# Kernel tuning notes

Measured on AMD Instinct MI355X. Metric: run time of the kernel, lower is better.

The kernel has to match this reference:

```python
import jax, jax.numpy as jnp
import numpy as np
import math

B, S, D, H = 2, 2048, 1024, 16
DK = D // H


def setup_inputs() -> dict:
    key = jax.random.key(0)
    ks = jax.random.split(key, 10)
    sc = 1.0 / math.sqrt(D)
    inp = {
        "Q_input": jax.random.normal(ks[0], (B, S, D), dtype=jnp.float32),
        "Wq_w": jax.random.normal(ks[1], (D, D), dtype=jnp.float32) * sc,
        "Wq_b": jnp.zeros((D,), dtype=jnp.float32),
        "Wk_w": jax.random.normal(ks[2], (D, D), dtype=jnp.float32) * sc,
        "Wk_b": jnp.zeros((D,), dtype=jnp.float32),
        "Wv_w": jax.random.normal(ks[3], (D, D), dtype=jnp.float32) * sc,
        "Wv_b": jnp.zeros((D,), dtype=jnp.float32),
        "Wo_w": jax.random.normal(ks[4], (D, D), dtype=jnp.float32) * sc,
        "Wo_b": jnp.zeros((D,), dtype=jnp.float32),
        # causal mask, broadcast over batch and heads: [1,1,S,S]
        "mask": jnp.tril(jnp.ones((S, S), dtype=jnp.int32))[None, None],
    }
    return inp


def reference(Q_input, Wq_w, Wq_b, Wk_w, Wk_b, Wv_w, Wv_b, Wo_w, Wo_b, mask):
    b, s, _ = Q_input.shape
    # linear projections (torch Linear: x @ W^T + b)
    Q = Q_input @ Wq_w.T + Wq_b
    K = Q_input @ Wk_w.T + Wk_b
    V = Q_input @ Wv_w.T + Wv_b
    # [b, h, s, dk]
    Q = Q.reshape(b, s, H, DK).transpose(0, 2, 1, 3)
    K = K.reshape(b, s, H, DK).transpose(0, 2, 1, 3)
    V = V.reshape(b, s, H, DK).transpose(0, 2, 1, 3)
    scores = jnp.einsum("bhqd,bhkd->bhqk", Q, K) / math.sqrt(DK)
    scores = jnp.where(mask == 0, jnp.float32(-1e9), scores)
    weights = jax.nn.softmax(scores, axis=-1)
    attn = jnp.einsum("bhqk,bhkd->bhqd", weights, V)
    attn = attn.transpose(0, 2, 1, 3).reshape(b, s, D)
    return attn @ Wo_w.T + Wo_b
```

## Files before the change

### kernel.cpp

```cpp
#include <hip/hip_runtime.h>
#include <hip/hip_bf16.h>
#include <cstdint>

typedef __attribute__((ext_vector_type(8))) short short8;
typedef __attribute__((ext_vector_type(4))) float f32x4;
typedef __attribute__((ext_vector_type(2))) unsigned int uint2v;
typedef unsigned short ushort_t;

#define S_LEN 2048
#define D_DIM 1024
#define NH 16
#define DK 64
#define BATCH 2
#define M_ROWS (BATCH * S_LEN)
#define BK 32

__device__ inline ushort_t f2bf(float f) {
    union { float f; uint32_t u; } v; v.f = f;
    uint32_t r = v.u + 0x7fffu + ((v.u >> 16) & 1u);
    return (ushort_t)(r >> 16);
}

__device__ __forceinline__ ushort_t bfc(float f) {
    __hip_bfloat16 h = __float2bfloat16(f);
    return __builtin_bit_cast(ushort_t, h);
}

__device__ __forceinline__ float bf2f(ushort_t u) {
    return __uint_as_float(((uint32_t)u) << 16);
}

__device__ __forceinline__ float fexp2(float x) {
#if __has_builtin(__builtin_amdgcn_exp2f)
    return __builtin_amdgcn_exp2f(x);
#else
    return exp2f(x);
#endif
}
__device__ __forceinline__ float frcp(float x) {
#if __has_builtin(__builtin_amdgcn_rcpf)
    return __builtin_amdgcn_rcpf(x);
#else
    return 1.0f / x;
#endif
}

__device__ __forceinline__ void glds16(const ushort_t* g, ushort_t* l) {
    __builtin_amdgcn_global_load_lds(
        (const __attribute__((address_space(1))) uint32_t*)g,
        (__attribute__((address_space(3))) uint32_t*)l,
        16, 0, 0);
}

#if __has_builtin(__builtin_amdgcn_permlane16_swap) && __has_builtin(__builtin_amdgcn_permlane32_swap)
#define HAS_PLSWAP 1
#else
#define HAS_PLSWAP 0
#endif

__device__ __forceinline__ float red_max4(float x) {
#if HAS_PLSWAP
    uint2v a = __builtin_amdgcn_permlane16_swap(__float_as_uint(x), __float_as_uint(x), false, false);
    float y = fmaxf(__uint_as_float(a.x), __uint_as_float(a.y));
    uint2v b = __builtin_amdgcn_permlane32_swap(__float_as_uint(y), __float_as_uint(y), false, false);
    return fmaxf(__uint_as_float(b.x), __uint_as_float(b.y));
#else
    x = fmaxf(x, __shfl_xor(x, 16));
    return fmaxf(x, __shfl_xor(x, 32));
#endif
}
__device__ __forceinline__ float red_sum4(float x) {
#if HAS_PLSWAP
    uint2v a = __builtin_amdgcn_permlane16_swap(__float_as_uint(x), __float_as_uint(x), false, false);
    float y = __uint_as_float(a.x) + __uint_as_float(a.y);
    uint2v b = __builtin_amdgcn_permlane32_swap(__float_as_uint(y), __float_as_uint(y), false, false);
    return __uint_as_float(b.x) + __uint_as_float(b.y);
#else
    x += __shfl_xor(x, 16);
    return x + __shfl_xor(x, 32);
#endif
}

__device__ __forceinline__ void route_p(const uint32_t wp[4][2], int ks, int lane, uint32_t F[4]) {
#if HAS_PLSWAP
    uint32_t U0 = wp[2 * ks][0],     U1 = wp[2 * ks][1];
    uint32_t V0 = wp[2 * ks + 1][0], V1 = wp[2 * ks + 1][1];
    uint2v t, pa0, pa1, pb0, pb1;
    t = __builtin_amdgcn_permlane32_swap(U0, U0, false, false);
    pa0 = __builtin_amdgcn_permlane16_swap(U0, t.y, false, false);
    t = __builtin_amdgcn_permlane32_swap(U1, U1, false, false);
    pa1 = __builtin_amdgcn_permlane16_swap(U1, t.y, false, false);
    t = __builtin_amdgcn_permlane32_swap(V0, V0, false, false);
    pb0 = __builtin_amdgcn_permlane16_swap(t.x, V0, false, false);
    t = __builtin_amdgcn_permlane32_swap(V1, V1, false, false);
    pb1 = __builtin_amdgcn_permlane16_swap(t.x, V1, false, false);
    bool lo = lane < 32;
    F[0] = lo ? pa0.x : pb0.x;
    F[1] = lo ? pa1.x : pb1.x;
    F[2] = lo ? pa0.y : pb0.y;
    F[3] = lo ? pa1.y : pb1.y;
#else
    int q = lane & 15, g = lane >> 4;
#pragma unroll
    for (int m = 0; m < 4; m++) {
        int src = 16 * (2 * (g & 1) + (m >> 1)) + q;
        uint32_t xa = (uint32_t)__shfl((int)wp[2 * ks][m & 1], src);
        uint32_t xb = (uint32_t)__shfl((int)wp[2 * ks + 1][m & 1], src);
        F[m] = (g < 2) ? xa : xb;
    }
#endif
}

__global__ void cvt_bf16(const float* __restrict__ in, ushort_t* __restrict__ out, int n4) {
    int i = blockIdx.x * blockDim.x + threadIdx.x;
    int stride = gridDim.x * blockDim.x;
    for (int idx = i; idx < n4; idx += stride) {
        float4 v = ((const float4*)in)[idx];
        ushort4 o;
        o.x = f2bf(v.x); o.y = f2bf(v.y); o.z = f2bf(v.z); o.w = f2bf(v.w);
        ((ushort4*)out)[idx] = o;
    }
}

__global__ void cvt_w3(const float* __restrict__ wq, const float* __restrict__ wk,
                       const float* __restrict__ wv, ushort_t* __restrict__ wqkv) {
    const int seg = (D_DIM * D_DIM) / 4;
    int i = blockIdx.x * blockDim.x + threadIdx.x;
    int stride = gridDim.x * blockDim.x;
    for (int idx = i; idx < 3 * seg; idx += stride) {
        int sel = idx >> 18;
        int id = idx & (seg - 1);
        const float* src = sel == 0 ? wq : (sel == 1 ? wk : wv);
        float4 v = ((const float4*)src)[id];
        ushort4 o;
        o.x = f2bf(v.x); o.y = f2bf(v.y); o.z = f2bf(v.z); o.w = f2bf(v.w);
        ((ushort4*)wqkv)[sel * seg + id] = o;
    }
}

template<int MODE, int BMt, int BNt>
__global__ __launch_bounds__(256) void gemm_bt(const ushort_t* __restrict__ A,
                                               const ushort_t* __restrict__ Bw,
                                               const float* __restrict__ b0,
                                               const float* __restrict__ b1,
                                               const float* __restrict__ b2,
                                               void* __restrict__ C0,
                                               void* __restrict__ C1,
                                               void* __restrict__ C2,
                                               int M, int N, int K) {
    constexpr int FM = BMt / 32, FN = BNt / 32;
    constexpr int ACH = BMt / 64, BCH = BNt / 64;
    __shared__ ushort_t As[BMt * BK];
    __shared__ ushort_t Bs[BNt * BK];
    int tid = threadIdx.x;
    int lane = tid & 63;
    int w = tid >> 6;
    int wr = w >> 1, wc = w & 1;
    int nwg = gridDim.x;
    int bx = (blockIdx.x & 7) * (nwg >> 3) + (blockIdx.x >> 3);
    int ntile = N / BNt;
    int m0 = (bx / ntile) * BMt;
    int n0 = (bx % ntile) * BNt;
    int lr = lane & 15;
    int lk = (lane >> 4) * 8;
    int srow = lane >> 2;
    int scol = (lane & 3) * 8;

    f32x4 acc[FM][FN] = {};

    for (int kt = 0; kt < K; kt += BK) {
        __syncthreads();
#pragma unroll
        for (int c = 0; c < ACH; c++)
            glds16(&A[(size_t)(m0 + w * (BMt / 4) + c * 16 + srow) * K + kt + scol],
                   &As[(w * (BMt / 4) + c * 16) * BK]);
#pragma unroll
        for (int c = 0; c < BCH; c++)
            glds16(&Bw[(size_t)(n0 + w * (BNt / 4) + c * 16 + srow) * K + kt + scol],
                   &Bs[(w * (BNt / 4) + c * 16) * BK]);
        __syncthreads();

        short8 af[FM], bf[FN];
#pragma unroll
        for (int f = 0; f < FM; f++)
            af[f] = *(const short8*)&As[(wr * (BMt / 2) + f * 16 + lr) * BK + lk];
#pragma unroll
        for (int f = 0; f < FN; f++)
            bf[f] = *(const short8*)&Bs[(wc * (BNt / 2) + f * 16 + lr) * BK + lk];
#pragma unroll
        for (int i = 0; i < FM; i++)
#pragma unroll
            for (int j = 0; j < FN; j++)
                acc[i][j] = __builtin_amdgcn_mfma_f32_16x16x32_bf16(af[i], bf[j], acc[i][j], 0, 0, 0);
    }

    int r0 = (lane >> 4) * 4;
#pragma unroll
    for (int j = 0; j < FN; j++) {
        int ncol = n0 + wc * (BNt / 2) + j * 16 + lr;
        if (MODE == 2) {
            float bv = b0[ncol];
#pragma unroll
            for (int i = 0; i < FM; i++) {
                int mbase = m0 + wr * (BMt / 2) + i * 16 + r0;
#pragma unroll
                for (int r = 0; r < 4; r++)
                    ((float*)C0)[(size_t)(mbase + r) * N + ncol] = acc[i][j][r] + bv;
            }
        } else {
            int sel = n0 >> 10;
            const float* bp = sel == 0 ? b0 : (sel == 1 ? b1 : b2);
            int nc = ncol & 1023;
            float bv = bp[nc];
            int hh = nc >> 6, dk = nc & 63;
            ushort_t* Co = (ushort_t*)(sel == 0 ? C0 : (sel == 1 ? C1 : C2));
#pragma unroll
            for (int i = 0; i < FM; i++) {
                int mbase = m0 + wr * (BMt / 2) + i * 16 + r0;
                int bb = mbase >> 11, ss = mbase & 2047;
                if (sel == 2) {
                    ushort4 pk;
                    pk.x = f2bf(acc[i][j][0] + bv);
                    pk.y = f2bf(acc[i][j][1] + bv);
                    pk.z = f2bf(acc[i][j][2] + bv);
                    pk.w = f2bf(acc[i][j][3] + bv);
                    size_t idx = ((size_t)(bb * NH + hh) * DK + dk) * S_LEN + ss;
                    *(ushort4*)&Co[idx] = pk;
                } else {
#pragma unroll
                    for (int r = 0; r < 4; r++) {
                        size_t idx = ((size_t)(bb * NH + hh) * S_LEN + (ss + r)) * DK + dk;
                        Co[idx] = f2bf(acc[i][j][r] + bv);
                    }
                }
            }
        }
    }
}

#define CSC 0.1803368801f

__device__ const unsigned char JTAB[40] = {
    23,22,21,20,19,18,17,16,
    31,31,30,28,29,26,27,15,
    24,25,30,28,29,27,26,14,
    24,11, 9,10, 8,25,12,13,
     0, 1, 2, 4, 6, 5, 7, 3};
__device__ const unsigned char KTAB[40] = {
     9, 9, 9, 9, 9, 9, 9, 9,
     0, 1, 0, 0, 0, 0, 1, 9,
     0, 0, 1, 1, 1, 0, 1, 9,
     1, 9, 9, 9, 9, 1, 9, 9,
     9, 9, 9, 9, 9, 9, 9, 9};

__global__ __launch_bounds__(256) void attn_fwd(const ushort_t* __restrict__ Q,
                                                const ushort_t* __restrict__ K,
                                                const ushort_t* __restrict__ Vt,
                                                ushort_t* __restrict__ Oa,
                                                float2* __restrict__ ml,
                                                float* __restrict__ Pd) {
    __shared__ ushort_t Ks[2][64 * 64];
    __shared__ ushort_t Vs[2][64 * 64];

    int tid = threadIdx.x;
    int lane = tid & 63;
    int w = tid >> 6;
    int bh = blockIdx.x;
    int yy = blockIdx.y;
    int j = JTAB[yy];
    int kk = KTAB[yy];
    int nt = j + 1;
    int half = (nt + 1) >> 1;
    int t0 = (kk == 1) ? half : 0;
    int t1 = (kk == 0) ? half : nt;
    int cnt = t1 - t0;
    int off = yy % cnt;
    size_t base = (size_t)bh * S_LEN * DK;
    int q0 = j * 64;

    int lr = lane & 15;
    int lk = (lane >> 4) * 8;
    int g16 = (lane >> 4) * 16;
    int r0 = (lane >> 4) * 4;
    int wq = w * 16 + lr;

    auto swz = [](int row, int cb) { return (row * 128 + (cb ^ ((row & 7) << 4))) >> 1; };

    short8 qf0 = *(const short8*)&Q[base + (size_t)(q0 + wq) * DK + lk];
    short8 qf1 = *(const short8*)&Q[base + (size_t)(q0 + wq) * DK + 32 + lk];

    f32x4 o[4] = {};
    float mrowL = -1e30f, lrow = 0.f;

    int sr = tid >> 3;
    int scb = (tid & 7) * 16;
    int sce = (tid & 7) * 8;

    {
        int tf = t0 + off;
        *(uint4*)&Ks[0][swz(sr, scb)]      = *(const uint4*)&K [base + (size_t)(tf * 64 + sr) * DK + sce];
        *(uint4*)&Ks[0][swz(sr + 32, scb)] = *(const uint4*)&K [base + (size_t)(tf * 64 + sr + 32) * DK + sce];
        *(uint4*)&Vs[0][swz(sr, scb)]      = *(const uint4*)&Vt[base + (size_t)sr * S_LEN + tf * 64 + sce];
        *(uint4*)&Vs[0][swz(sr + 32, scb)] = *(const uint4*)&Vt[base + (size_t)(sr + 32) * S_LEN + tf * 64 + sce];
    }
    __syncthreads();

    int cur = 0;
    for (int s = 0; s < cnt; ++s) {
        int to = s + off; if (to >= cnt) to -= cnt;
        int t = t0 + to;
        bool last = (s == cnt - 1);
        bool diag = (t == j);
        uint4 kr0, kr1, vr0, vr1;
        if (!last) {
            int tno = s + 1 + off; if (tno >= cnt) tno -= cnt;
            int tn = t0 + tno;
            kr0 = *(const uint4*)&K [base + (size_t)(tn * 64 + sr) * DK + sce];
            kr1 = *(const uint4*)&K [base + (size_t)(tn * 64 + sr + 32) * DK + sce];
            vr0 = *(const uint4*)&Vt[base + (size_t)sr * S_LEN + tn * 64 + sce];
            vr1 = *(const uint4*)&Vt[base + (size_t)(sr + 32) * S_LEN + tn * 64 + sce];
        }

        f32x4 st[4] = {};
        __builtin_amdgcn_s_setprio(1);
#pragma unroll
        for (int n = 0; n < 4; n++) {
            if (!diag || n <= w) {
                short8 kf0 = *(const short8*)&Ks[cur][swz(n * 16 + lr, g16)];
                short8 kf1 = *(const short8*)&Ks[cur][swz(n * 16 + lr, 64 + g16)];
                st[n] = __builtin_amdgcn_mfma_f32_16x16x32_bf16(kf0, qf0, st[n], 0, 0, 0);
                st[n] = __builtin_amdgcn_mfma_f32_16x16x32_bf16(kf1, qf1, st[n], 0, 0, 0);
            }
        }
        __builtin_amdgcn_s_setprio(0);

        if (diag) {
#pragma unroll
            for (int n = 0; n < 4; n++)
#pragma unroll
                for (int i = 0; i < 4; i++)
                    if (16 * n + r0 + i > wq) st[n][i] = -1e30f;
        }

        float m0 = fmaxf(fmaxf(fmaxf(st[0][0], st[0][1]), st[0][2]), st[0][3]);
        float m1 = fmaxf(fmaxf(fmaxf(st[1][0], st[1][1]), st[1][2]), st[1][3]);
        float m2 = fmaxf(fmaxf(fmaxf(st[2][0], st[2][1]), st[2][2]), st[2][3]);
        float m3 = fmaxf(fmaxf(fmaxf(st[3][0], st[3][1]), st[3][2]), st[3][3]);
        float mx = fmaxf(fmaxf(fmaxf(m0, m1), m2), m3);
        float mxL = red_max4(mx) * CSC;

        bool skip = __all(mxL <= mrowL + 8.0f);
        float corr = 1.0f;
        float mnewL = mrowL;
        if (!skip) {
            mnewL = fmaxf(mrowL, mxL);
            corr = fexp2(mrowL - mnewL);
            mrowL = mnewL;
        }

        float psum = 0.f;
        uint32_t wp[4][2];
#pragma unroll
        for (int n = 0; n < 4; n++) {
#pragma unroll
            for (int i = 0; i < 4; i++) {
                float p = fexp2(fmaf(st[n][i], CSC, -mnewL));
                st[n][i] = p;
                psum += p;
            }
            wp[n][0] = (uint32_t)bfc(st[n][0]) | ((uint32_t)bfc(st[n][1]) << 16);
            wp[n][1] = (uint32_t)bfc(st[n][2]) | ((uint32_t)bfc(st[n][3]) << 16);
        }
        psum = red_sum4(psum);

        if (skip) {
            lrow += psum;
        } else {
            lrow = lrow * corr + psum;
            float cb[4];
#pragma unroll
            for (int i = 0; i < 4; i++) cb[i] = __shfl(corr, r0 + i);
#pragma unroll
            for (int d = 0; d < 4; d++)
#pragma unroll
                for (int i = 0; i < 4; i++) o[d][i] *= cb[i];
        }

#pragma unroll
        for (int ks = 0; ks < 2; ks++) {
            if (diag && 32 * ks > w * 16 + 15) continue;
            uint32_t F[4];
            route_p(wp, ks, lane, F);
            union { uint32_t u[4]; short8 s; } pu;
            pu.u[0] = F[0]; pu.u[1] = F[1]; pu.u[2] = F[2]; pu.u[3] = F[3];
            short8 pf = pu.s;
            __builtin_amdgcn_s_setprio(1);
#pragma unroll
            for (int d = 0; d < 4; d++) {
                short8 vf = *(const short8*)&Vs[cur][swz(d * 16 + lr, ks * 64 + g16)];
                o[d] = __builtin_amdgcn_mfma_f32_16x16x32_bf16(pf, vf, o[d], 0, 0, 0);
            }
            __builtin_amdgcn_s_setprio(0);
        }

        if (!last) {
            *(uint4*)&Ks[cur ^ 1][swz(sr, scb)]      = kr0;
            *(uint4*)&Ks[cur ^ 1][swz(sr + 32, scb)] = kr1;
            *(uint4*)&Vs[cur ^ 1][swz(sr, scb)]      = vr0;
            *(uint4*)&Vs[cur ^ 1][swz(sr + 32, scb)] = vr1;
        }
        __syncthreads();
        cur ^= 1;
    }

    int b = bh >> 4, h = bh & 15;
    if (kk == 9) {
        float lb[4];
#pragma unroll
        for (int i = 0; i < 4; i++) lb[i] = frcp(__shfl(lrow, r0 + i));
#pragma unroll
        for (int d = 0; d < 4; d++)
#pragma unroll
            for (int i = 0; i < 4; i++) {
                int qq = q0 + w * 16 + r0 + i;
                int dk = d * 16 + lr;
                size_t idx = ((size_t)(b * S_LEN + qq)) * D_DIM + h * DK + dk;
                Oa[idx] = bfc(o[d][i] * lb[i]);
            }
    } else {
        int jj = j - 24;
        if (kk == 0) {
#pragma unroll
            for (int d = 0; d < 4; d++)
#pragma unroll
                for (int i = 0; i < 4; i++) {
                    int qq = q0 + w * 16 + r0 + i;
                    int dk = d * 16 + lr;
                    size_t idx = ((size_t)(b * S_LEN + qq)) * D_DIM + h * DK + dk;
                    Oa[idx] = bfc(o[d][i]);
                }
        } else {
#pragma unroll
            for (int d = 0; d < 4; d++)
#pragma unroll
                for (int i = 0; i < 4; i++) {
                    int rloc = w * 16 + r0 + i;
                    Pd[((size_t)(bh * 8 + jj) * 64 + rloc) * 64 + d * 16 + lr] = o[d][i];
                }
        }
        if (lane < 16) {
            int row = w * 16 + lane;
            ml[(size_t)kk * 16384 + (bh * 8 + jj) * 64 + row] = make_float2(mrowL, lrow);
        }
    }
}

__global__ __launch_bounds__(256) void attn_merge(const float2* __restrict__ ml,
                                                  const float* __restrict__ Pd,
                                                  ushort_t* __restrict__ Oa) {
    int bh = blockIdx.x;
    int jj = blockIdx.y;
    int tid = threadIdx.x;
    int r = tid >> 2;
    int q = (tid & 3) * 16;
    int b = bh >> 4, h = bh & 15;
    int row = (jj + 24) * 64 + r;
    float2 a = ml[(bh * 8 + jj) * 64 + r];
    float2 c = ml[16384 + (bh * 8 + jj) * 64 + r];
    float M = fmaxf(a.x, c.x);
    float w0 = fexp2(a.x - M), w1 = fexp2(c.x - M);
    float rc = frcp(a.y * w0 + c.y * w1);
    size_t ob = ((size_t)(b * S_LEN + row)) * D_DIM + h * DK + q;
    const float* p1 = &Pd[((size_t)(bh * 8 + jj) * 64 + r) * 64 + q];
#pragma unroll
    for (int i = 0; i < 4; i++) {
        ushort4 o0 = *(const ushort4*)&Oa[ob + i * 4];
        float4 o1 = *(const float4*)&p1[i * 4];
        ushort4 res;
        res.x = bfc((bf2f(o0.x) * w0 + o1.x * w1) * rc);
        res.y = bfc((bf2f(o0.y) * w0 + o1.y * w1) * rc);
        res.z = bfc((bf2f(o0.z) * w0 + o1.z * w1) * rc);
        res.w = bfc((bf2f(o0.w) * w0 + o1.w * w1) * rc);
        *(ushort4*)&Oa[ob + i * 4] = res;
    }
}

extern "C" void kernel_launch(void* const* d_in, const int* in_sizes, int n_in,
                              void* d_out, int out_size, void* d_ws, size_t ws_size,
                              hipStream_t stream) {
    const float* X  = (const float*)d_in[0];
    const float* Wq = (const float*)d_in[1];
    const float* bq = (const float*)d_in[2];
    const float* Wk = (const float*)d_in[3];
    const float* bk = (const float*)d_in[4];
    const float* Wv = (const float*)d_in[5];
    const float* bv = (const float*)d_in[6];
    const float* Wo = (const float*)d_in[7];
    const float* bo = (const float*)d_in[8];
    float* out = (float*)d_out;

    char* ws = (char*)d_ws;
    ushort_t* Xb    = (ushort_t*)ws;
    ushort_t* Wqkvb = (ushort_t*)(ws + (8u  << 20));
    float2*   mlbuf = (float2*)(ws + (8u  << 20));
    ushort_t* Qb    = (ushort_t*)(ws + (14u << 20));
    ushort_t* Kb    = (ushort_t*)(ws + (22u << 20));
    ushort_t* Vtb   = (ushort_t*)(ws + (30u << 20));
    ushort_t* Wob   = Wqkvb;
    ushort_t* Ab    = Xb;
    float*    Pd    = out;

    const int M = M_ROWS;
    int nX4 = (M * D_DIM) / 4;
    int nW4 = (D_DIM * D_DIM) / 4;

    cvt_bf16<<<2048, 256, 0, stream>>>(X, Xb, nX4);
    cvt_w3<<<2048, 256, 0, stream>>>(Wq, Wk, Wv, Wqkvb);

    gemm_bt<3, 128, 128><<<dim3((M / 128) * (3072 / 128)), 256, 0, stream>>>(
        Xb, Wqkvb, bq, bk, bv, Qb, Kb, Vtb, M, 3072, D_DIM);

    dim3 agrid(BATCH * NH, 40);
    attn_fwd<<<agrid, 256, 0, stream>>>(Qb, Kb, Vtb, Ab, mlbuf, Pd);

    attn_merge<<<dim3(BATCH * NH, 8), 256, 0, stream>>>(mlbuf, Pd, Ab);

    cvt_bf16<<<2048, 256, 0, stream>>>(Wo, Wob, nW4);

    gemm_bt<2, 64, 128><<<dim3((M / 64) * (D_DIM / 128)), 256, 0, stream>>>(
        Ab, Wob, bo, bo, bo, out, out, out, M, D_DIM, D_DIM);
}
```

Measured before the change: 126.8 us.

## Double-buffer GEMM shared tiles, add occupancy hints, strength-reduce attention prefetch addressing

The projection GEMM now uses two shared-memory buffers. It issues the global-to-LDS load for the next K slice before computing on the current one, which removes one barrier per iteration and overlaps loads with MFMA work. Both kernels get minimum-occupancy hints in launch_bounds, (256,3) and (256,5), which may force the compiler to cap registers. The attention kernel's K/V prefetch addressing is rewritten as incrementally advanced pointers with a wrap, replacing per-iteration modulo index arithmetic. Risks are extra LDS use in the GEMM and register spills under the tighter bounds.

Measured after the change: 119.1 us. -6.1%, faster.

```diff
diff --git a/kernel.cpp b/kernel.cpp
--- a/kernel.cpp
+++ b/kernel.cpp
@@ -139,19 +139,19 @@
 }
 
 template<int MODE, int BMt, int BNt>
-__global__ __launch_bounds__(256) void gemm_bt(const ushort_t* __restrict__ A,
-                                               const ushort_t* __restrict__ Bw,
-                                               const float* __restrict__ b0,
-                                               const float* __restrict__ b1,
-                                               const float* __restrict__ b2,
-                                               void* __restrict__ C0,
-                                               void* __restrict__ C1,
-                                               void* __restrict__ C2,
-                                               int M, int N, int K) {
+__global__ __launch_bounds__(256, 3) void gemm_bt(const ushort_t* __restrict__ A,
+                                                  const ushort_t* __restrict__ Bw,
+                                                  const float* __restrict__ b0,
+                                                  const float* __restrict__ b1,
+                                                  const float* __restrict__ b2,
+                                                  void* __restrict__ C0,
+                                                  void* __restrict__ C1,
+                                                  void* __restrict__ C2,
+                                                  int M, int N, int K) {
     constexpr int FM = BMt / 32, FN = BNt / 32;
     constexpr int ACH = BMt / 64, BCH = BNt / 64;
-    __shared__ ushort_t As[BMt * BK];
-    __shared__ ushort_t Bs[BNt * BK];
+    __shared__ ushort_t As[2][BMt * BK];
+    __shared__ ushort_t Bs[2][BNt * BK];
     int tid = threadIdx.x;
     int lane = tid & 63;
     int w = tid >> 6;
@@ -166,32 +166,40 @@
     int srow = lane >> 2;
     int scol = (lane & 3) * 8;
 
-    f32x4 acc[FM][FN] = {};
-
-    for (int kt = 0; kt < K; kt += BK) {
-        __syncthreads();
+    auto stage = [&](int b, int kt) {
 #pragma unroll
         for (int c = 0; c < ACH; c++)
             glds16(&A[(size_t)(m0 + w * (BMt / 4) + c * 16 + srow) * K + kt + scol],
-                   &As[(w * (BMt / 4) + c * 16) * BK]);
+                   &As[b][(w * (BMt / 4) + c * 16) * BK]);
 #pragma unroll
         for (int c = 0; c < BCH; c++)
             glds16(&Bw[(size_t)(n0 + w * (BNt / 4) + c * 16 + srow) * K + kt + scol],
-                   &Bs[(w * (BNt / 4) + c * 16) * BK]);
-        __syncthreads();
+                   &Bs[b][(w * (BNt / 4) + c * 16) * BK]);
+    };
+
+    f32x4 acc[FM][FN] = {};
+
+    stage(0, 0);
+    __syncthreads();
+    int cur = 0;
+    for (int kt = 0; kt < K; kt += BK) {
+        if (kt + BK < K) stage(cur ^ 1, kt + BK);
 
         short8 af[FM], bf[FN];
 #pragma unroll
         for (int f = 0; f < FM; f++)
-            af[f] = *(const short8*)&As[(wr * (BMt / 2) + f * 16 + lr) * BK + lk];
+            af[f] = *(const short8*)&As[cur][(wr * (BMt / 2) + f * 16 + lr) * BK + lk];
 #pragma unroll
         for (int f = 0; f < FN; f++)
-            bf[f] = *(const short8*)&Bs[(wc * (BNt / 2) + f * 16 + lr) * BK + lk];
+            bf[f] = *(const short8*)&Bs[cur][(wc * (BNt / 2) + f * 16 + lr) * BK + lk];
 #pragma unroll
         for (int i = 0; i < FM; i++)
 #pragma unroll
             for (int j = 0; j < FN; j++)
                 acc[i][j] = __builtin_amdgcn_mfma_f32_16x16x32_bf16(af[i], bf[j], acc[i][j], 0, 0, 0);
+
+        __syncthreads();
+        cur ^= 1;
     }
 
     int r0 = (lane >> 4) * 4;
@@ -253,12 +261,12 @@
      1, 9, 9, 9, 9, 1, 9, 9,
      9, 9, 9, 9, 9, 9, 9, 9};
 
-__global__ __launch_bounds__(256) void attn_fwd(const ushort_t* __restrict__ Q,
-                                                const ushort_t* __restrict__ K,
-                                                const ushort_t* __restrict__ Vt,
-                                                ushort_t* __restrict__ Oa,
-                                                float2* __restrict__ ml,
-                                                float* __restrict__ Pd) {
+__global__ __launch_bounds__(256, 5) void attn_fwd(const ushort_t* __restrict__ Q,
+                                                   const ushort_t* __restrict__ K,
+                                                   const ushort_t* __restrict__ Vt,
+                                                   ushort_t* __restrict__ Oa,
+                                                   float2* __restrict__ ml,
+                                                   float* __restrict__ Pd) {
     __shared__ ushort_t Ks[2][64 * 64];
     __shared__ ushort_t Vs[2][64 * 64];
 
@@ -296,29 +304,35 @@
     int scb = (tid & 7) * 16;
     int sce = (tid & 7) * 8;
 
+    const ushort_t* kBase = K  + base + (size_t)sr * DK + sce;
+    const ushort_t* vBase = Vt + base + (size_t)sr * S_LEN + sce;
+
+    int tf = t0 + off;
     {
-        int tf = t0 + off;
-        *(uint4*)&Ks[0][swz(sr, scb)]      = *(const uint4*)&K [base + (size_t)(tf * 64 + sr) * DK + sce];
-        *(uint4*)&Ks[0][swz(sr + 32, scb)] = *(const uint4*)&K [base + (size_t)(tf * 64 + sr + 32) * DK + sce];
-        *(uint4*)&Vs[0][swz(sr, scb)]      = *(const uint4*)&Vt[base + (size_t)sr * S_LEN + tf * 64 + sce];
-        *(uint4*)&Vs[0][swz(sr + 32, scb)] = *(const uint4*)&Vt[base + (size_t)(sr + 32) * S_LEN + tf * 64 + sce];
+        const ushort_t* kp = kBase + (size_t)tf * (64 * DK);
+        const ushort_t* vp = vBase + (size_t)tf * 64;
+        *(uint4*)&Ks[0][swz(sr, scb)]      = *(const uint4*)kp;
+        *(uint4*)&Ks[0][swz(sr + 32, scb)] = *(const uint4*)(kp + 32 * DK);
+        *(uint4*)&Vs[0][swz(sr, scb)]      = *(const uint4*)vp;
+        *(uint4*)&Vs[0][swz(sr + 32, scb)] = *(const uint4*)(vp + 32 * S_LEN);
     }
     __syncthreads();
+
+    int t = tf;
+    int tpre = (tf == t1 - 1) ? t0 : tf + 1;
+    const ushort_t* kPre = kBase + (size_t)tpre * (64 * DK);
+    const ushort_t* vPre = vBase + (size_t)tpre * 64;
 
     int cur = 0;
     for (int s = 0; s < cnt; ++s) {
-        int to = s + off; if (to >= cnt) to -= cnt;
-        int t = t0 + to;
         bool last = (s == cnt - 1);
         bool diag = (t == j);
         uint4 kr0, kr1, vr0, vr1;
         if (!last) {
-            int tno = s + 1 + off; if (tno >= cnt) tno -= cnt;
-            int tn = t0 + tno;
-            kr0 = *(const uint4*)&K [base + (size_t)(tn * 64 + sr) * DK + sce];
-            kr1 = *(const uint4*)&K [base + (size_t)(tn * 64 + sr + 32) * DK + sce];
-            vr0 = *(const uint4*)&Vt[base + (size_t)sr * S_LEN + tn * 64 + sce];
-            vr1 = *(const uint4*)&Vt[base + (size_t)(sr + 32) * S_LEN + tn * 64 + sce];
+            kr0 = *(const uint4*)kPre;
+            kr1 = *(const uint4*)(kPre + 32 * DK);
+            vr0 = *(const uint4*)vPre;
+            vr1 = *(const uint4*)(vPre + 32 * S_LEN);
         }
 
         f32x4 st[4] = {};
@@ -411,6 +425,12 @@
         }
         __syncthreads();
         cur ^= 1;
+
+        t = tpre;
+        bool wrap = (tpre == t1 - 1);
+        tpre = wrap ? t0 : tpre + 1;
+        kPre += wrap ? -(ptrdiff_t)(cnt - 1) * (64 * DK) : (ptrdiff_t)(64 * DK);
+        vPre += wrap ? -(ptrdiff_t)(cnt - 1) * 64 : (ptrdiff_t)64;
     }
 
     int b = bh >> 4, h = bh & 15;
```
